# Kernel optimization log

Measured on AMD Instinct MI355X. Metric: run time of the kernel, lower is better.

## Reference

```python
import jax, jax.numpy as jnp
import numpy as np

N, E, F, H, C, K, L, B = 50000, 800000, 64, 64, 10, 4, 3, 256


def setup_inputs() -> dict:
    key = jax.random.key(0)
    ks = jax.random.split(key, 24)
    nrm = lambda k, s, sc=0.1: jax.random.normal(k, s, jnp.float32) * sc
    inp = {}
    inp['x'] = jax.random.normal(ks[0], (N, F), jnp.float32)
    inp['edge_index'] = jax.random.randint(ks[1], (2, E), 0, N)
    inp['batch'] = jnp.sort(jax.random.randint(ks[2], (N,), 0, B))
    i = 3
    for pre in ('ce', 'cl'):  # causal encoder / classifier encoder (GIN, F==H)
        inp[pre + '_W1'] = nrm(ks[i], (L, H, H)); inp[pre + '_b1'] = jnp.zeros((L, H), jnp.float32)
        inp[pre + '_W2'] = nrm(ks[i + 1], (L, H, H)); inp[pre + '_b2'] = jnp.zeros((L, H), jnp.float32)
        inp[pre + '_eps'] = jnp.zeros((L,), jnp.float32)
        i += 2
    inp['nm_W1'] = nrm(ks[i], (K, H, H)); inp['nm_b1'] = jnp.zeros((K, H), jnp.float32)
    inp['nm_W2'] = nrm(ks[i + 1], (K, H, 1)); inp['nm_b2'] = jnp.zeros((K, 1), jnp.float32)
    inp['em_W1'] = nrm(ks[i + 2], (K, 2 * H, H)); inp['em_b1'] = jnp.zeros((K, H), jnp.float32)
    inp['em_W2'] = nrm(ks[i + 3], (K, H, 1)); inp['em_b2'] = jnp.zeros((K, 1), jnp.float32)
    inp['fm_W1'] = nrm(ks[i + 4], (K, H, H)); inp['fm_b1'] = jnp.zeros((K, H), jnp.float32)
    inp['fm_W2'] = nrm(ks[i + 5], (K, H, F)); inp['fm_b2'] = jnp.zeros((K, F), jnp.float32)
    inp['clf_W'] = nrm(ks[i + 6], (K, H, C)); inp['clf_b'] = jnp.zeros((K, C), jnp.float32)
    return inp


def _gin(h, src, dst, W1, b1, W2, b2, eps, ew=None):
    """GIN with edge weights: h' = MLP((1+eps)*h + sum_j w_ij * h_j), ReLU after each conv."""
    n = h.shape[0]
    for l in range(W1.shape[0]):
        m = h[src]                                   # [E, H] gather
        if ew is not None:
            m = m * ew[:, None]
        agg = jax.ops.segment_sum(m, dst, num_segments=n)  # scatter-add
        t = (1.0 + eps[l]) * h + agg
        h = jax.nn.relu(jax.nn.relu(t @ W1[l] + b1[l]) @ W2[l] + b2[l])
    return h


def _mlp2(z, W1, b1, W2, b2):
    # z: [n, d]; per-expert 2-layer MLP -> [K, n, out]
    hdn = jax.nn.relu(jnp.einsum('nd,kdh->knh', z, W1) + b1[:, None, :])
    return jnp.einsum('knh,kho->kno', hdn, W2) + b2[:, None, :]


def _mean_pool(z, batch, nseg):
    s = jax.ops.segment_sum(z, batch, num_segments=nseg)
    cnt = jax.ops.segment_sum(jnp.ones((z.shape[-2],), z.dtype), batch, num_segments=nseg)
    return s / jnp.maximum(cnt, 1.0)[:, None]


def reference(x, edge_index, batch,
              ce_W1, ce_b1, ce_W2, ce_b2, ce_eps,
              cl_W1, cl_b1, cl_W2, cl_b2, cl_eps,
              nm_W1, nm_b1, nm_W2, nm_b2,
              em_W1, em_b1, em_W2, em_b2,
              fm_W1, fm_b1, fm_W2, fm_b2,
              clf_W, clf_b):
    src, dst = edge_index[0], edge_index[1]
    Z = _gin(x, src, dst, ce_W1, ce_b1, ce_W2, ce_b2, ce_eps)          # [N, H]
    edge_feat = jnp.concatenate([Z[src], Z[dst]], axis=1)              # [E, 2H]

    node_masks = jax.nn.sigmoid(_mlp2(Z, nm_W1, nm_b1, nm_W2, nm_b2))  # [K, N, 1]
    edge_masks = jax.nn.sigmoid(_mlp2(edge_feat, em_W1, em_b1, em_W2, em_b2))  # [K, E, 1]
    feat_masks = jax.nn.sigmoid(_mlp2(Z, fm_W1, fm_b1, fm_W2, fm_b2))  # [K, N, F]

    masked_x = x[None] * node_masks * feat_masks                       # [K, N, F]
    ew = edge_masks[..., 0]                                            # [K, E]

    masked_Z = jax.vmap(
        lambda h0, w: _gin(h0, src, dst, cl_W1, cl_b1, cl_W2, cl_b2, cl_eps, ew=w)
    )(masked_x, ew)                                                    # [K, N, H]

    h_stable = jax.vmap(lambda z: _mean_pool(z, batch, B))(masked_Z)   # [K, B, H]
    expert_logits = jnp.einsum('kbh,khc->kbc', h_stable, clf_W) + clf_b[:, None, :]
    h_orig = _mean_pool(Z, batch, B)                                   # [B, H]

    # match torch's stack(dim=1) layouts
    return (jnp.transpose(expert_logits, (1, 0, 2)),   # [B, K, C]
            jnp.transpose(h_stable, (1, 0, 2)),        # [B, K, H]
            h_orig,                                    # [B, H]
            jnp.transpose(node_masks, (1, 0, 2)),      # [N, K, 1]
            jnp.transpose(edge_masks, (1, 0, 2)),      # [E, K, 1]
            jnp.transpose(feat_masks, (1, 0, 2)))      # [N, K, F]
```

## Files before the change

kernel.cpp:

```cpp
#include <hip/hip_runtime.h>
#include <math.h>

#define N_NODES 50000
#define N_EDGES 800000
#define DIM 64
#define NB 256
#define NK 4
#define NC 10
#define TPAD 68
#define SCAN_BLKS 196

typedef unsigned int uint_;
typedef unsigned short ushort_;

__device__ __forceinline__ float sigmoidf_(float x){ return 1.f/(1.f+__expf(-x)); }
__device__ __forceinline__ float bf2f(ushort_ v){ return __uint_as_float(((uint_)v)<<16); }
__device__ __forceinline__ float bflo(uint_ u){ return __uint_as_float(u<<16); }
__device__ __forceinline__ float bfhi(uint_ u){ return __uint_as_float(u & 0xFFFF0000u); }
__device__ __forceinline__ ushort_ f2bf(float f){
    uint_ u = __float_as_uint(f);
    u = (u + 0x7FFFu + ((u>>16)&1u)) >> 16;
    return (ushort_)u;
}

__global__ void deg_hist_kernel(const int* __restrict__ ei, int* __restrict__ deg){
    int e = blockIdx.x*256 + threadIdx.x;
    if (e < N_EDGES) atomicAdd(&deg[ei[N_EDGES + e]], 1);
}

__global__ __launch_bounds__(256)
void scan_p1(const int* __restrict__ deg, int* __restrict__ rowptr, int* __restrict__ bsum){
    __shared__ int s[256];
    int tid = threadIdx.x;
    int i = blockIdx.x*256 + tid;
    int v = (i < N_NODES) ? deg[i] : 0;
    s[tid] = v;
    __syncthreads();
    for (int off = 1; off < 256; off <<= 1){
        int t = (tid >= off) ? s[tid - off] : 0;
        __syncthreads();
        s[tid] += t;
        __syncthreads();
    }
    if (i < N_NODES) rowptr[i] = s[tid] - v;
    if (tid == 255) bsum[blockIdx.x] = s[255];
}

__global__ __launch_bounds__(256)
void scan_p2(const int* __restrict__ bsum, int* __restrict__ boff){
    __shared__ int s[256];
    int tid = threadIdx.x;
    int v = (tid < SCAN_BLKS) ? bsum[tid] : 0;
    s[tid] = v;
    __syncthreads();
    for (int off = 1; off < 256; off <<= 1){
        int t = (tid >= off) ? s[tid - off] : 0;
        __syncthreads();
        s[tid] += t;
        __syncthreads();
    }
    boff[tid] = s[tid] - v;
}

__global__ __launch_bounds__(256)
void scan_p3(int* __restrict__ rowptr, const int* __restrict__ boff, int* __restrict__ cursor){
    int i = blockIdx.x*256 + threadIdx.x;
    if (i < N_NODES){
        int r = rowptr[i] + boff[blockIdx.x];
        rowptr[i] = r;
        cursor[i] = r;
    }
    if (i == 0) rowptr[N_NODES] = N_EDGES;
}

__global__ void csr_fill_kernel(const int* __restrict__ ei, int* __restrict__ cursor,
                                int* __restrict__ csr_src, int* __restrict__ csr_eid){
    int e = blockIdx.x*256 + threadIdx.x;
    if (e < N_EDGES){
        int d = ei[N_EDGES + e];
        int pos = atomicAdd(&cursor[d], 1);
        csr_src[pos] = ei[e];
        csr_eid[pos] = e;
    }
}

__global__ void tobf16_kernel(const float* __restrict__ x, ushort_* __restrict__ o){
    int i = blockIdx.x*256 + threadIdx.x;
    if (i < N_NODES*DIM/4){
        float4 v = *(const float4*)&x[(size_t)i*4];
        ushort4 o4;
        o4.x = f2bf(v.x); o4.y = f2bf(v.y); o4.z = f2bf(v.z); o4.w = f2bf(v.w);
        *(ushort4*)&o[(size_t)i*4] = o4;
    }
}

__global__ __launch_bounds__(256)
void agg_ce_kernel(const ushort_* __restrict__ hin, float* __restrict__ outt,
                   const int* __restrict__ rowptr, const int* __restrict__ csr_src,
                   const float* __restrict__ eps_p)
{
    const int n = blockIdx.x*4 + (threadIdx.x >> 6);
    if (n >= N_NODES) return;
    const int lane = threadIdx.x & 63;
    const int f2 = lane & 31;
    const int p  = lane >> 5;
    float a0 = 0.f, a1 = 0.f;
    int idx = rowptr[n];
    const int end = rowptr[n+1];
    for (; idx + 4 <= end; idx += 4){
        int e0 = idx + p*2, e1 = e0 + 1;
        int s0 = csr_src[e0], s1 = csr_src[e1];
        uint_ g0 = *(const uint_*)&hin[(size_t)s0*DIM + f2*2];
        uint_ g1 = *(const uint_*)&hin[(size_t)s1*DIM + f2*2];
        a0 += bflo(g0) + bflo(g1);
        a1 += bfhi(g0) + bfhi(g1);
    }
    for (; idx < end; idx += 2){
        int e = idx + p;
        bool v = e < end;
        int s = v ? csr_src[e] : 0;
        uint_ g = v ? *(const uint_*)&hin[(size_t)s*DIM + f2*2] : 0u;
        a0 += bflo(g);
        a1 += bfhi(g);
    }
    a0 += __shfl_xor(a0, 32);
    a1 += __shfl_xor(a1, 32);
    const float epv = 1.0f + *eps_p;
    uint_ hs = *(const uint_*)&hin[(size_t)n*DIM + f2*2];
    a0 = fmaf(epv, bflo(hs), a0);
    a1 = fmaf(epv, bfhi(hs), a1);
    if (p == 0){
        *(float2*)&outt[(size_t)n*DIM + f2*2] = make_float2(a0, a1);
    }
}

__global__ __launch_bounds__(256)
void agg4_kernel(const ushort_* __restrict__ h4, ushort_* __restrict__ out4,
                 const int* __restrict__ rowptr, const int* __restrict__ csr_src,
                 const ushort_* __restrict__ ewi, const float* __restrict__ eps_p)
{
    const int n = blockIdx.x*4 + (threadIdx.x >> 6);
    if (n >= N_NODES) return;
    const int lane = threadIdx.x & 63;
    const int k = lane >> 4;
    const float epv = 1.0f + *eps_p;
    uint2 self = *(const uint2*)&h4[(size_t)n*(NK*DIM) + lane*4];
    float c0 = epv*bflo(self.x), c1 = epv*bfhi(self.x);
    float c2 = epv*bflo(self.y), c3 = epv*bfhi(self.y);
    int idx = rowptr[n];
    const int end = rowptr[n+1];
    for (; idx + 4 <= end; idx += 4){
        int s0 = csr_src[idx+0], s1 = csr_src[idx+1];
        int s2 = csr_src[idx+2], s3 = csr_src[idx+3];
        uint2 g0 = *(const uint2*)&h4[(size_t)s0*(NK*DIM) + lane*4];
        uint2 g1 = *(const uint2*)&h4[(size_t)s1*(NK*DIM) + lane*4];
        uint2 g2 = *(const uint2*)&h4[(size_t)s2*(NK*DIM) + lane*4];
        uint2 g3 = *(const uint2*)&h4[(size_t)s3*(NK*DIM) + lane*4];
        float w0 = bf2f(ewi[(size_t)(idx+0)*NK + k]);
        float w1 = bf2f(ewi[(size_t)(idx+1)*NK + k]);
        float w2 = bf2f(ewi[(size_t)(idx+2)*NK + k]);
        float w3 = bf2f(ewi[(size_t)(idx+3)*NK + k]);
        c0 = fmaf(w0, bflo(g0.x), c0); c1 = fmaf(w0, bfhi(g0.x), c1);
        c2 = fmaf(w0, bflo(g0.y), c2); c3 = fmaf(w0, bfhi(g0.y), c3);
        c0 = fmaf(w1, bflo(g1.x), c0); c1 = fmaf(w1, bfhi(g1.x), c1);
        c2 = fmaf(w1, bflo(g1.y), c2); c3 = fmaf(w1, bfhi(g1.y), c3);
        c0 = fmaf(w2, bflo(g2.x), c0); c1 = fmaf(w2, bfhi(g2.x), c1);
        c2 = fmaf(w2, bflo(g2.y), c2); c3 = fmaf(w2, bfhi(g2.y), c3);
        c0 = fmaf(w3, bflo(g3.x), c0); c1 = fmaf(w3, bfhi(g3.x), c1);
        c2 = fmaf(w3, bflo(g3.y), c2); c3 = fmaf(w3, bfhi(g3.y), c3);
    }
    for (; idx < end; ++idx){
        int s = csr_src[idx];
        uint2 g = *(const uint2*)&h4[(size_t)s*(NK*DIM) + lane*4];
        float w = bf2f(ewi[(size_t)idx*NK + k]);
        c0 = fmaf(w, bflo(g.x), c0); c1 = fmaf(w, bfhi(g.x), c1);
        c2 = fmaf(w, bflo(g.y), c2); c3 = fmaf(w, bfhi(g.y), c3);
    }
    ushort4 o;
    o.x = f2bf(c0); o.y = f2bf(c1); o.z = f2bf(c2); o.w = f2bf(c3);
    *(ushort4*)&out4[(size_t)n*(NK*DIM) + lane*4] = o;
}

__device__ __forceinline__ void load_tileT_f32s(const float* __restrict__ in, float As[DIM][TPAD],
                                                int m0, int tid, int istride, int ibase){
    int r = tid >> 2, cq = (tid & 3) * 16;
    bool valid = (m0 + r) < N_NODES;
#pragma unroll
    for (int i = 0; i < 4; i++){
        float4 v = valid ? *(const float4*)&in[(size_t)(m0 + r)*istride + ibase + cq + 4*i]
                         : make_float4(0.f, 0.f, 0.f, 0.f);
        As[cq + 4*i + 0][r] = v.x;
        As[cq + 4*i + 1][r] = v.y;
        As[cq + 4*i + 2][r] = v.z;
        As[cq + 4*i + 3][r] = v.w;
    }
}

__device__ __forceinline__ void load_tileT_b16s(const ushort_* __restrict__ in, float As[DIM][TPAD],
                                                int m0, int tid, int istride, int ibase){
    int r = tid >> 2, cq = (tid & 3) * 16;
    bool valid = (m0 + r) < N_NODES;
    uint_ us[8] = {0,0,0,0,0,0,0,0};
    if (valid){
        const uint_* p = (const uint_*)&in[(size_t)(m0 + r)*istride + ibase + cq];
        uint4 a = *(const uint4*)p;
        uint4 b = *(const uint4*)(p + 4);
        us[0]=a.x; us[1]=a.y; us[2]=a.z; us[3]=a.w;
        us[4]=b.x; us[5]=b.y; us[6]=b.z; us[7]=b.w;
    }
#pragma unroll
    for (int w = 0; w < 8; w++){
        As[cq + 2*w + 0][r] = bflo(us[w]);
        As[cq + 2*w + 1][r] = bfhi(us[w]);
    }
}

__device__ __forceinline__ void load_w(const float* __restrict__ W, float Ws[DIM][TPAD], int tid){
    int kr = tid >> 2, cq = (tid & 3) * 16;
#pragma unroll
    for (int i = 0; i < 4; i++){
        *(float4*)&Ws[kr][cq + 4*i] = *(const float4*)&W[(size_t)kr*DIM + cq + 4*i];
    }
}

template<int IN16, int ACT2, int OUT16, int PERK_W>
__global__ __launch_bounds__(256)
void mlpX_kernel(const void* __restrict__ inp, void* __restrict__ outp,
                 const float* __restrict__ W1, const float* __restrict__ b1,
                 const float* __restrict__ W2, const float* __restrict__ b2,
                 int istride, int ibase_k, int ostride, int obase_k)
{
    __shared__ __align__(16) float As[DIM][TPAD];
    __shared__ __align__(16) float Ws[DIM][TPAD];
    __shared__ __align__(16) float Ts[DIM][TPAD];
    const int tid = threadIdx.x;
    const int tx = tid & 15, ty = tid >> 4;
    const int m0 = blockIdx.x * 64;
    const int k = blockIdx.y;
    if (PERK_W){
        W1 += (size_t)k*DIM*DIM; b1 += (size_t)k*DIM;
        W2 += (size_t)k*DIM*DIM; b2 += (size_t)k*DIM;
    }
    const int ibase = k * ibase_k;
    const size_t obase = (size_t)k * obase_k;

    if (IN16) load_tileT_b16s((const ushort_*)inp, As, m0, tid, istride, ibase);
    else      load_tileT_f32s((const float*)inp, As, m0, tid, istride, ibase);
    load_w(W1, Ws, tid);
    __syncthreads();

    float acc[4][4];
    {
        float4 b1v = *(const float4*)&b1[tx*4];
        float bv[4] = {b1v.x, b1v.y, b1v.z, b1v.w};
#pragma unroll
        for (int i = 0; i < 4; i++)
#pragma unroll
            for (int j = 0; j < 4; j++) acc[i][j] = bv[j];
    }
#pragma unroll 8
    for (int kk = 0; kk < DIM; kk++){
        float4 a = *(const float4*)&As[kk][ty*4];
        float4 w = *(const float4*)&Ws[kk][tx*4];
        float av[4] = {a.x, a.y, a.z, a.w};
        float wv[4] = {w.x, w.y, w.z, w.w};
#pragma unroll
        for (int i = 0; i < 4; i++)
#pragma unroll
            for (int j = 0; j < 4; j++) acc[i][j] = fmaf(av[i], wv[j], acc[i][j]);
    }
#pragma unroll
    for (int j = 0; j < 4; j++){
        float4 v = make_float4(fmaxf(acc[0][j],0.f), fmaxf(acc[1][j],0.f),
                               fmaxf(acc[2][j],0.f), fmaxf(acc[3][j],0.f));
        *(float4*)&Ts[tx*4 + j][ty*4] = v;
    }
    __syncthreads();
    load_w(W2, Ws, tid);
    __syncthreads();

    float acc2[4][4];
    {
        float4 b2v = *(const float4*)&b2[tx*4];
        float bv[4] = {b2v.x, b2v.y, b2v.z, b2v.w};
#pragma unroll
        for (int i = 0; i < 4; i++)
#pragma unroll
            for (int j = 0; j < 4; j++) acc2[i][j] = bv[j];
    }
#pragma unroll 8
    for (int kk = 0; kk < DIM; kk++){
        float4 a = *(const float4*)&Ts[kk][ty*4];
        float4 w = *(const float4*)&Ws[kk][tx*4];
        float av[4] = {a.x, a.y, a.z, a.w};
        float wv[4] = {w.x, w.y, w.z, w.w};
#pragma unroll
        for (int i = 0; i < 4; i++)
#pragma unroll
            for (int j = 0; j < 4; j++) acc2[i][j] = fmaf(av[i], wv[j], acc2[i][j]);
    }
#pragma unroll
    for (int i = 0; i < 4; i++){
        int m = m0 + ty*4 + i;
        if (m < N_NODES){
            float v0, v1, v2, v3;
            if (ACT2 == 0){
                v0 = fmaxf(acc2[i][0],0.f); v1 = fmaxf(acc2[i][1],0.f);
                v2 = fmaxf(acc2[i][2],0.f); v3 = fmaxf(acc2[i][3],0.f);
            } else {
                v0 = sigmoidf_(acc2[i][0]); v1 = sigmoidf_(acc2[i][1]);
                v2 = sigmoidf_(acc2[i][2]); v3 = sigmoidf_(acc2[i][3]);
            }
            if (OUT16){
                ushort4 o;
                o.x = f2bf(v0); o.y = f2bf(v1); o.z = f2bf(v2); o.w = f2bf(v3);
                *(ushort4*)&((ushort_*)outp)[obase + (size_t)m*ostride + tx*4] = o;
            } else {
                *(float4*)&((float*)outp)[obase + (size_t)m*ostride + tx*4] =
                    make_float4(v0, v1, v2, v3);
            }
        }
    }
}

__global__ __launch_bounds__(256)
void nm4_kernel(const ushort_* __restrict__ Z16, float* __restrict__ nm_out,
                const float* __restrict__ nmW1, const float* __restrict__ nmb1,
                const float* __restrict__ nmW2, const float* __restrict__ nmb2)
{
    __shared__ __align__(16) float As[DIM][TPAD];
    __shared__ __align__(16) float Ws[DIM][TPAD];
    __shared__ __align__(16) float Ts[DIM][TPAD];
    __shared__ float w2s[DIM];
    __shared__ float red[4][DIM];
    const int tid = threadIdx.x;
    const int tx = tid & 15, ty = tid >> 4;
    const int m0 = blockIdx.x * 64;
    const int k = blockIdx.y;
    const float* W1 = nmW1 + (size_t)k*DIM*DIM;
    const float* b1 = nmb1 + (size_t)k*DIM;
    const float* w2 = nmW2 + (size_t)k*DIM;

    load_tileT_b16s(Z16, As, m0, tid, DIM, 0);
    load_w(W1, Ws, tid);
    if (tid < DIM) w2s[tid] = w2[tid];
    __syncthreads();

    float acc[4][4];
    {
        float4 b1v = *(const float4*)&b1[tx*4];
        float bv[4] = {b1v.x, b1v.y, b1v.z, b1v.w};
#pragma unroll
        for (int i = 0; i < 4; i++)
#pragma unroll
            for (int j = 0; j < 4; j++) acc[i][j] = bv[j];
    }
#pragma unroll 8
    for (int kk = 0; kk < DIM; kk++){
        float4 a = *(const float4*)&As[kk][ty*4];
        float4 w = *(const float4*)&Ws[kk][tx*4];
        float av[4] = {a.x, a.y, a.z, a.w};
        float wv[4] = {w.x, w.y, w.z, w.w};
#pragma unroll
        for (int i = 0; i < 4; i++)
#pragma unroll
            for (int j = 0; j < 4; j++) acc[i][j] = fmaf(av[i], wv[j], acc[i][j]);
    }
#pragma unroll
    for (int j = 0; j < 4; j++){
        float4 v = make_float4(fmaxf(acc[0][j],0.f), fmaxf(acc[1][j],0.f),
                               fmaxf(acc[2][j],0.f), fmaxf(acc[3][j],0.f));
        *(float4*)&Ts[tx*4 + j][ty*4] = v;
    }
    __syncthreads();
    {
        int m = tid & 63, q = tid >> 6;
        float p = 0.f;
#pragma unroll
        for (int kk = 0; kk < 16; kk++) p = fmaf(Ts[q*16 + kk][m], w2s[q*16 + kk], p);
        red[q][m] = p;
    }
    __syncthreads();
    if (tid < DIM){
        int m = m0 + tid;
        if (m < N_NODES){
            float sm = red[0][tid] + red[1][tid] + red[2][tid] + red[3][tid] + nmb2[k];
            nm_out[(size_t)m*NK + k] = sigmoidf_(sm);
        }
    }
}

__global__ __launch_bounds__(256)
void em_proj4_kernel(const ushort_* __restrict__ Z16, const float* __restrict__ emW1,
                     ushort_* __restrict__ pt4, ushort_* __restrict__ pb4)
{
    __shared__ __align__(16) float As[DIM][TPAD];
    __shared__ __align__(16) float Ws[DIM][TPAD];
    const int s = blockIdx.y;
    const int k = s >> 1, side = s & 1;
    const float* W = emW1 + ((size_t)k*2 + side)*DIM*DIM;
    ushort_* outp = side ? pb4 : pt4;
    const int tid = threadIdx.x;
    const int tx = tid & 15, ty = tid >> 4;
    const int m0 = blockIdx.x * 64;

    load_tileT_b16s(Z16, As, m0, tid, DIM, 0);
    load_w(W, Ws, tid);
    __syncthreads();

    float acc[4][4] = {};
#pragma unroll 8
    for (int kk = 0; kk < DIM; kk++){
        float4 a = *(const float4*)&As[kk][ty*4];
        float4 w = *(const float4*)&Ws[kk][tx*4];
        float av[4] = {a.x, a.y, a.z, a.w};
        float wv[4] = {w.x, w.y, w.z, w.w};
#pragma unroll
        for (int i = 0; i < 4; i++)
#pragma unroll
            for (int j = 0; j < 4; j++) acc[i][j] = fmaf(av[i], wv[j], acc[i][j]);
    }
#pragma unroll
    for (int i = 0; i < 4; i++){
        int m = m0 + ty*4 + i;
        if (m < N_NODES){
            ushort4 o;
            o.x = f2bf(acc[i][0]); o.y = f2bf(acc[i][1]);
            o.z = f2bf(acc[i][2]); o.w = f2bf(acc[i][3]);
            *(ushort4*)&outp[(size_t)m*(NK*DIM) + k*DIM + tx*4] = o;
        }
    }
}

__global__ __launch_bounds__(256)
void edge_mask16_kernel(const ushort_* __restrict__ pt4, const ushort_* __restrict__ pb4,
                        const int* __restrict__ rowptr, const int* __restrict__ csr_src,
                        const int* __restrict__ csr_eid,
                        const float* __restrict__ emb1, const float* __restrict__ emW2,
                        const float* __restrict__ emb2,
                        float* __restrict__ em_out, ushort_* __restrict__ ewi)
{
    const int n = blockIdx.x*4 + (threadIdx.x >> 6);
    if (n >= N_NODES) return;
    const int lane = threadIdx.x & 63;
    const int k = lane >> 4, fq = lane & 15;
    const float4 w2v = *(const float4*)&emW2[k*DIM + fq*4];
    const float4 b1v = *(const float4*)&emb1[k*DIM + fq*4];
    const float b2 = emb2[k];
    uint2 pbu = *(const uint2*)&pb4[(size_t)n*(NK*DIM) + k*DIM + fq*4];
    const float pre0 = bflo(pbu.x) + b1v.x;
    const float pre1 = bfhi(pbu.x) + b1v.y;
    const float pre2 = bflo(pbu.y) + b1v.z;
    const float pre3 = bfhi(pbu.y) + b1v.w;
    int i = rowptr[n];
    const int end = rowptr[n+1];
    for (; i + 2 <= end; i += 2){
        int s0 = csr_src[i], s1 = csr_src[i+1];
        uint2 a0 = *(const uint2*)&pt4[(size_t)s0*(NK*DIM) + k*DIM + fq*4];
        uint2 a1 = *(const uint2*)&pt4[(size_t)s1*(NK*DIM) + k*DIM + fq*4];
        float p0 = fmaxf(bflo(a0.x) + pre0, 0.f)*w2v.x + fmaxf(bfhi(a0.x) + pre1, 0.f)*w2v.y
                 + fmaxf(bflo(a0.y) + pre2, 0.f)*w2v.z + fmaxf(bfhi(a0.y) + pre3, 0.f)*w2v.w;
        float p1 = fmaxf(bflo(a1.x) + pre0, 0.f)*w2v.x + fmaxf(bfhi(a1.x) + pre1, 0.f)*w2v.y
                 + fmaxf(bflo(a1.y) + pre2, 0.f)*w2v.z + fmaxf(bfhi(a1.y) + pre3, 0.f)*w2v.w;
        p0 += __shfl_xor(p0, 1, 16); p1 += __shfl_xor(p1, 1, 16);
        p0 += __shfl_xor(p0, 2, 16); p1 += __shfl_xor(p1, 2, 16);
        p0 += __shfl_xor(p0, 4, 16); p1 += __shfl_xor(p1, 4, 16);
        p0 += __shfl_xor(p0, 8, 16); p1 += __shfl_xor(p1, 8, 16);
        if (fq == 0){
            float m0v = sigmoidf_(p0 + b2);
            float m1v = sigmoidf_(p1 + b2);
            em_out[(size_t)csr_eid[i]*NK + k]   = m0v;
            em_out[(size_t)csr_eid[i+1]*NK + k] = m1v;
            ewi[(size_t)i*NK + k]     = f2bf(m0v);
            ewi[(size_t)(i+1)*NK + k] = f2bf(m1v);
        }
    }
    for (; i < end; ++i){
        int s0 = csr_src[i];
        uint2 a0 = *(const uint2*)&pt4[(size_t)s0*(NK*DIM) + k*DIM + fq*4];
        float p0 = fmaxf(bflo(a0.x) + pre0, 0.f)*w2v.x + fmaxf(bfhi(a0.x) + pre1, 0.f)*w2v.y
                 + fmaxf(bflo(a0.y) + pre2, 0.f)*w2v.z + fmaxf(bfhi(a0.y) + pre3, 0.f)*w2v.w;
        p0 += __shfl_xor(p0, 1, 16);
        p0 += __shfl_xor(p0, 2, 16);
        p0 += __shfl_xor(p0, 4, 16);
        p0 += __shfl_xor(p0, 8, 16);
        if (fq == 0){
            float m0v = sigmoidf_(p0 + b2);
            em_out[(size_t)csr_eid[i]*NK + k] = m0v;
            ewi[(size_t)i*NK + k] = f2bf(m0v);
        }
    }
}

__global__ void build_h04_kernel(const float* __restrict__ x, const float* __restrict__ nm_out,
                                 const float* __restrict__ fm_out, ushort_* __restrict__ h4)
{
    int t = blockIdx.x*256 + threadIdx.x;
    if (t < N_NODES*64){
        int n = t >> 6;
        int q = t & 63;
        int k = q >> 4, c = (q & 15) * 4;
        float nm = nm_out[(size_t)n*NK + k];
        float4 xv = *(const float4*)&x[(size_t)n*DIM + c];
        float4 fv = *(const float4*)&fm_out[((size_t)n*NK + k)*DIM + c];
        ushort4 o;
        o.x = f2bf(xv.x*nm*fv.x); o.y = f2bf(xv.y*nm*fv.y);
        o.z = f2bf(xv.z*nm*fv.z); o.w = f2bf(xv.w*nm*fv.w);
        *(ushort4*)&h4[(size_t)n*(NK*DIM) + k*DIM + c] = o;
    }
}

__device__ __forceinline__ int lower_bound_(const int* a, int n, int v){
    int lo = 0, hi = n;
    while (lo < hi){ int m = (lo + hi) >> 1; if (a[m] < v) lo = m + 1; else hi = m; }
    return lo;
}

__global__ __launch_bounds__(64)
void pool_orig_kernel(const ushort_* __restrict__ h, const int* __restrict__ batch, float* __restrict__ out){
    int b = blockIdx.x, lane = threadIdx.x;
    int lo = lower_bound_(batch, N_NODES, b);
    int hi = lower_bound_(batch, N_NODES, b+1);
    float s = 0.f;
    int n = lo;
    for (; n + 4 <= hi; n += 4){
        s += bf2f(h[(size_t)n*DIM + lane]) + bf2f(h[(size_t)(n+1)*DIM + lane])
           + bf2f(h[(size_t)(n+2)*DIM + lane]) + bf2f(h[(size_t)(n+3)*DIM + lane]);
    }
    for (; n < hi; ++n) s += bf2f(h[(size_t)n*DIM + lane]);
    out[(size_t)b*DIM + lane] = s / fmaxf((float)(hi - lo), 1.f);
}

__global__ __launch_bounds__(64)
void pool4_kernel(const ushort_* __restrict__ h4, const int* __restrict__ batch,
                  const float* __restrict__ clfW, const float* __restrict__ clfb,
                  float* __restrict__ out_logits, float* __restrict__ out_hst)
{
    __shared__ float ms[DIM];
    int b = blockIdx.x, k = blockIdx.y, lane = threadIdx.x;
    int lo = lower_bound_(batch, N_NODES, b);
    int hi = lower_bound_(batch, N_NODES, b+1);
    const ushort_* h = h4 + (size_t)k*DIM;
    float s = 0.f;
    int n = lo;
    for (; n + 4 <= hi; n += 4){
        s += bf2f(h[(size_t)n*(NK*DIM) + lane]) + bf2f(h[(size_t)(n+1)*(NK*DIM) + lane])
           + bf2f(h[(size_t)(n+2)*(NK*DIM) + lane]) + bf2f(h[(size_t)(n+3)*(NK*DIM) + lane]);
    }
    for (; n < hi; ++n) s += bf2f(h[(size_t)n*(NK*DIM) + lane]);
    float m = s / fmaxf((float)(hi - lo), 1.f);
    out_hst[((size_t)b*NK + k)*DIM + lane] = m;
    ms[lane] = m;
    __syncthreads();
    if (lane < NC){
        float a = clfb[(size_t)k*NC + lane];
        const float* W = clfW + (size_t)k*DIM*NC;
#pragma unroll
        for (int j = 0; j < DIM; j++) a = fmaf(ms[j], W[j*NC + lane], a);
        out_logits[((size_t)b*NK + k)*NC + lane] = a;
    }
}

extern "C" void kernel_launch(void* const* d_in, const int* in_sizes, int n_in,
                              void* d_out, int out_size, void* d_ws, size_t ws_size,
                              hipStream_t stream)
{
    const float* x     = (const float*)d_in[0];
    const int*   ei    = (const int*)  d_in[1];
    const int*   batch = (const int*)  d_in[2];
    const float* ceW1 = (const float*)d_in[3];
    const float* ceb1 = (const float*)d_in[4];
    const float* ceW2 = (const float*)d_in[5];
    const float* ceb2 = (const float*)d_in[6];
    const float* ceeps= (const float*)d_in[7];
    const float* clW1 = (const float*)d_in[8];
    const float* clb1 = (const float*)d_in[9];
    const float* clW2 = (const float*)d_in[10];
    const float* clb2 = (const float*)d_in[11];
    const float* cleps= (const float*)d_in[12];
    const float* nmW1 = (const float*)d_in[13];
    const float* nmb1 = (const float*)d_in[14];
    const float* nmW2 = (const float*)d_in[15];
    const float* nmb2 = (const float*)d_in[16];
    const float* emW1 = (const float*)d_in[17];
    const float* emb1 = (const float*)d_in[18];
    const float* emW2 = (const float*)d_in[19];
    const float* emb2 = (const float*)d_in[20];
    const float* fmW1 = (const float*)d_in[21];
    const float* fmb1 = (const float*)d_in[22];
    const float* fmW2 = (const float*)d_in[23];
    const float* fmb2 = (const float*)d_in[24];
    const float* clfW = (const float*)d_in[25];
    const float* clfb = (const float*)d_in[26];

    float* out        = (float*)d_out;
    float* out_logits = out;
    float* out_hst    = out + 10240;
    float* out_horig  = out + 75776;
    float* nm_out     = out + 92160;
    float* em_out     = out + 292160;
    float* fm_out     = out + 3492160;

    int* rowptr  = (int*)d_ws;
    int* cursor  = rowptr + (N_NODES + 1);
    int* deg     = cursor + N_NODES;
    int* csr_src = deg + N_NODES;
    int* csr_eid = csr_src + N_EDGES;
    int* bsum    = csr_eid + N_EDGES;
    int* boff    = bsum + 256;
    size_t int_count = (size_t)(N_NODES+1) + N_NODES + N_NODES + N_EDGES + N_EDGES + 512;
    int_count = (int_count + 3) & ~(size_t)3;
    const size_t ND = (size_t)N_NODES*DIM;
    float*   tbuf = (float*)(((int*)d_ws) + int_count);
    ushort_* hx16 = (ushort_*)(tbuf + ND);
    ushort_* TA   = hx16 + ND;
    ushort_* h4A  = (ushort_*)tbuf;
    ushort_* TB   = TA + ND;
    ushort_* pt4  = TB + ND;
    ushort_* pb4  = pt4 + ND*NK;
    ushort_* ewi  = pb4 + ND*NK;
    ushort_* t16  = pt4;
    ushort_* h4B  = pb4;

    const int GT = (N_NODES + 63) / 64;
    const int GW = (N_NODES + 3) / 4;

    hipMemsetAsync(deg, 0, N_NODES*sizeof(int), stream);
    deg_hist_kernel<<<(N_EDGES+255)/256, 256, 0, stream>>>(ei, deg);
    scan_p1<<<SCAN_BLKS, 256, 0, stream>>>(deg, rowptr, bsum);
    scan_p2<<<1, 256, 0, stream>>>(bsum, boff);
    scan_p3<<<SCAN_BLKS, 256, 0, stream>>>(rowptr, boff, cursor);
    csr_fill_kernel<<<(N_EDGES+255)/256, 256, 0, stream>>>(ei, cursor, csr_src, csr_eid);

    tobf16_kernel<<<(N_NODES*DIM/4+255)/256, 256, 0, stream>>>(x, hx16);

    agg_ce_kernel<<<GW, 256, 0, stream>>>(hx16, tbuf, rowptr, csr_src, ceeps + 0);
    mlpX_kernel<0,0,1,0><<<dim3(GT,1), 256, 0, stream>>>(tbuf, TA, ceW1 + 0*DIM*DIM, ceb1 + 0*DIM,
                                                         ceW2 + 0*DIM*DIM, ceb2 + 0*DIM, DIM, 0, DIM, 0);
    agg_ce_kernel<<<GW, 256, 0, stream>>>(TA, tbuf, rowptr, csr_src, ceeps + 1);
    mlpX_kernel<0,0,1,0><<<dim3(GT,1), 256, 0, stream>>>(tbuf, TB, ceW1 + 1*DIM*DIM, ceb1 + 1*DIM,
                                                         ceW2 + 1*DIM*DIM, ceb2 + 1*DIM, DIM, 0, DIM, 0);
    agg_ce_kernel<<<GW, 256, 0, stream>>>(TB, tbuf, rowptr, csr_src, ceeps + 2);
    mlpX_kernel<0,0,1,0><<<dim3(GT,1), 256, 0, stream>>>(tbuf, TA, ceW1 + 2*DIM*DIM, ceb1 + 2*DIM,
                                                         ceW2 + 2*DIM*DIM, ceb2 + 2*DIM, DIM, 0, DIM, 0);
    const ushort_* Z16 = TA;

    pool_orig_kernel<<<NB, 64, 0, stream>>>(Z16, batch, out_horig);

    em_proj4_kernel<<<dim3(GT, 2*NK), 256, 0, stream>>>(Z16, emW1, pt4, pb4);
    edge_mask16_kernel<<<GW, 256, 0, stream>>>(pt4, pb4, rowptr, csr_src, csr_eid,
                                               emb1, emW2, emb2, em_out, ewi);

    nm4_kernel<<<dim3(GT, NK), 256, 0, stream>>>(Z16, nm_out, nmW1, nmb1, nmW2, nmb2);
    mlpX_kernel<1,1,0,1><<<dim3(GT, NK), 256, 0, stream>>>(Z16, fm_out, fmW1, fmb1, fmW2, fmb2,
                                                           DIM, 0, NK*DIM, DIM);

    build_h04_kernel<<<(N_NODES*64+255)/256, 256, 0, stream>>>(x, nm_out, fm_out, h4A);

    agg4_kernel<<<GW, 256, 0, stream>>>(h4A, t16, rowptr, csr_src, ewi, cleps + 0);
    mlpX_kernel<1,0,1,0><<<dim3(GT, NK), 256, 0, stream>>>(t16, h4B, clW1 + 0*DIM*DIM, clb1 + 0*DIM,
                                                           clW2 + 0*DIM*DIM, clb2 + 0*DIM,
                                                           NK*DIM, DIM, NK*DIM, DIM);
    agg4_kernel<<<GW, 256, 0, stream>>>(h4B, t16, rowptr, csr_src, ewi, cleps + 1);
    mlpX_kernel<1,0,1,0><<<dim3(GT, NK), 256, 0, stream>>>(t16, h4A, clW1 + 1*DIM*DIM, clb1 + 1*DIM,
                                                           clW2 + 1*DIM*DIM, clb2 + 1*DIM,
                                                           NK*DIM, DIM, NK*DIM, DIM);
    agg4_kernel<<<GW, 256, 0, stream>>>(h4A, t16, rowptr, csr_src, ewi, cleps + 2);
    mlpX_kernel<1,0,1,0><<<dim3(GT, NK), 256, 0, stream>>>(t16, h4B, clW1 + 2*DIM*DIM, clb1 + 2*DIM,
                                                           clW2 + 2*DIM*DIM, clb2 + 2*DIM,
                                                           NK*DIM, DIM, NK*DIM, DIM);

    pool4_kernel<<<dim3(NB, NK), 64, 0, stream>>>(h4B, batch, clfW, clfb, out_logits, out_hst);
}
```

Measured before the change: 995.4 us.

## Store gathered node features and edge projections in FP8 instead of BF16

The per-expert node features gathered by the classifier GIN aggregation, the edge-mask projection tables and the pooled final hidden states are now written as packed FP8 (four values per 32-bit word). They are unpacked with the hardware cvt_pk_f32_fp8 instructions. This halves the bytes moved by the random-access gathers in agg4 and edge_mask, which are likely bandwidth or latency bound. The trade-off is a large loss of precision (FP8 mantissa) in intermediate activations, which may break accuracy tolerance. The workspace layout is also reshuffled so h4B gets its own region.

```diff
diff --git a/kernel.cpp b/kernel.cpp
--- a/kernel.cpp
+++ b/kernel.cpp
@@ -12,6 +12,8 @@
 
 typedef unsigned int uint_;
 typedef unsigned short ushort_;
+typedef unsigned char uchar_;
+typedef float f32x2_ __attribute__((ext_vector_type(2)));
 
 __device__ __forceinline__ float sigmoidf_(float x){ return 1.f/(1.f+__expf(-x)); }
 __device__ __forceinline__ float bf2f(ushort_ v){ return __uint_as_float(((uint_)v)<<16); }
@@ -21,6 +23,13 @@
     uint_ u = __float_as_uint(f);
     u = (u + 0x7FFFu + ((u>>16)&1u)) >> 16;
     return (ushort_)u;
+}
+__device__ __forceinline__ f32x2_ fp8lo(uint_ u){ return __builtin_amdgcn_cvt_pk_f32_fp8(u, false); }
+__device__ __forceinline__ f32x2_ fp8hi(uint_ u){ return __builtin_amdgcn_cvt_pk_f32_fp8(u, true); }
+__device__ __forceinline__ uint_ pack_fp8x4(float a, float b, float c, float d){
+    uint_ u = __builtin_amdgcn_cvt_pk_fp8_f32(a, b, 0, false);
+    u = __builtin_amdgcn_cvt_pk_fp8_f32(c, d, u, true);
+    return u;
 }
 
 __global__ void deg_hist_kernel(const int* __restrict__ ei, int* __restrict__ deg){
@@ -135,7 +144,7 @@
 }
 
 __global__ __launch_bounds__(256)
-void agg4_kernel(const ushort_* __restrict__ h4, ushort_* __restrict__ out4,
+void agg4_kernel(const uint_* __restrict__ h4, ushort_* __restrict__ out4,
                  const int* __restrict__ rowptr, const int* __restrict__ csr_src,
                  const ushort_* __restrict__ ewi, const float* __restrict__ eps_p)
 {
@@ -144,37 +153,42 @@
     const int lane = threadIdx.x & 63;
     const int k = lane >> 4;
     const float epv = 1.0f + *eps_p;
-    uint2 self = *(const uint2*)&h4[(size_t)n*(NK*DIM) + lane*4];
-    float c0 = epv*bflo(self.x), c1 = epv*bfhi(self.x);
-    float c2 = epv*bflo(self.y), c3 = epv*bfhi(self.y);
+    uint_ self = h4[(size_t)n*64 + lane];
+    f32x2_ sl = fp8lo(self), sh = fp8hi(self);
+    float c0 = epv*sl.x, c1 = epv*sl.y, c2 = epv*sh.x, c3 = epv*sh.y;
     int idx = rowptr[n];
     const int end = rowptr[n+1];
     for (; idx + 4 <= end; idx += 4){
         int s0 = csr_src[idx+0], s1 = csr_src[idx+1];
         int s2 = csr_src[idx+2], s3 = csr_src[idx+3];
-        uint2 g0 = *(const uint2*)&h4[(size_t)s0*(NK*DIM) + lane*4];
-        uint2 g1 = *(const uint2*)&h4[(size_t)s1*(NK*DIM) + lane*4];
-        uint2 g2 = *(const uint2*)&h4[(size_t)s2*(NK*DIM) + lane*4];
-        uint2 g3 = *(const uint2*)&h4[(size_t)s3*(NK*DIM) + lane*4];
+        uint_ g0 = h4[(size_t)s0*64 + lane];
+        uint_ g1 = h4[(size_t)s1*64 + lane];
+        uint_ g2 = h4[(size_t)s2*64 + lane];
+        uint_ g3 = h4[(size_t)s3*64 + lane];
         float w0 = bf2f(ewi[(size_t)(idx+0)*NK + k]);
         float w1 = bf2f(ewi[(size_t)(idx+1)*NK + k]);
         float w2 = bf2f(ewi[(size_t)(idx+2)*NK + k]);
         float w3 = bf2f(ewi[(size_t)(idx+3)*NK + k]);
-        c0 = fmaf(w0, bflo(g0.x), c0); c1 = fmaf(w0, bfhi(g0.x), c1);
-        c2 = fmaf(w0, bflo(g0.y), c2); c3 = fmaf(w0, bfhi(g0.y), c3);
-        c0 = fmaf(w1, bflo(g1.x), c0); c1 = fmaf(w1, bfhi(g1.x), c1);
-        c2 = fmaf(w1, bflo(g1.y), c2); c3 = fmaf(w1, bfhi(g1.y), c3);
-        c0 = fmaf(w2, bflo(g2.x), c0); c1 = fmaf(w2, bfhi(g2.x), c1);
-        c2 = fmaf(w2, bflo(g2.y), c2); c3 = fmaf(w2, bfhi(g2.y), c3);
-        c0 = fmaf(w3, bflo(g3.x), c0); c1 = fmaf(w3, bfhi(g3.x), c1);
-        c2 = fmaf(w3, bflo(g3.y), c2); c3 = fmaf(w3, bfhi(g3.y), c3);
+        f32x2_ l0 = fp8lo(g0), h0v = fp8hi(g0);
+        f32x2_ l1 = fp8lo(g1), h1v = fp8hi(g1);
+        f32x2_ l2 = fp8lo(g2), h2v = fp8hi(g2);
+        f32x2_ l3 = fp8lo(g3), h3v = fp8hi(g3);
+        c0 = fmaf(w0, l0.x, c0); c1 = fmaf(w0, l0.y, c1);
+        c2 = fmaf(w0, h0v.x, c2); c3 = fmaf(w0, h0v.y, c3);
+        c0 = fmaf(w1, l1.x, c0); c1 = fmaf(w1, l1.y, c1);
+        c2 = fmaf(w1, h1v.x, c2); c3 = fmaf(w1, h1v.y, c3);
+        c0 = fmaf(w2, l2.x, c0); c1 = fmaf(w2, l2.y, c1);
+        c2 = fmaf(w2, h2v.x, c2); c3 = fmaf(w2, h2v.y, c3);
+        c0 = fmaf(w3, l3.x, c0); c1 = fmaf(w3, l3.y, c1);
+        c2 = fmaf(w3, h3v.x, c2); c3 = fmaf(w3, h3v.y, c3);
     }
     for (; idx < end; ++idx){
         int s = csr_src[idx];
-        uint2 g = *(const uint2*)&h4[(size_t)s*(NK*DIM) + lane*4];
+        uint_ g = h4[(size_t)s*64 + lane];
         float w = bf2f(ewi[(size_t)idx*NK + k]);
-        c0 = fmaf(w, bflo(g.x), c0); c1 = fmaf(w, bfhi(g.x), c1);
-        c2 = fmaf(w, bflo(g.y), c2); c3 = fmaf(w, bfhi(g.y), c3);
+        f32x2_ l = fp8lo(g), h = fp8hi(g);
+        c0 = fmaf(w, l.x, c0); c1 = fmaf(w, l.y, c1);
+        c2 = fmaf(w, h.x, c2); c3 = fmaf(w, h.y, c3);
     }
     ushort4 o;
     o.x = f2bf(c0); o.y = f2bf(c1); o.z = f2bf(c2); o.w = f2bf(c3);
@@ -223,7 +237,7 @@
     }
 }
 
-template<int IN16, int ACT2, int OUT16, int PERK_W>
+template<int IN16, int ACT2, int OUTMODE, int PERK_W>
 __global__ __launch_bounds__(256)
 void mlpX_kernel(const void* __restrict__ inp, void* __restrict__ outp,
                  const float* __restrict__ W1, const float* __restrict__ b1,
@@ -311,10 +325,13 @@
                 v0 = sigmoidf_(acc2[i][0]); v1 = sigmoidf_(acc2[i][1]);
                 v2 = sigmoidf_(acc2[i][2]); v3 = sigmoidf_(acc2[i][3]);
             }
-            if (OUT16){
+            if (OUTMODE == 1){
                 ushort4 o;
                 o.x = f2bf(v0); o.y = f2bf(v1); o.z = f2bf(v2); o.w = f2bf(v3);
                 *(ushort4*)&((ushort_*)outp)[obase + (size_t)m*ostride + tx*4] = o;
+            } else if (OUTMODE == 2){
+                uint_ u = pack_fp8x4(v0, v1, v2, v3);
+                ((uint_*)outp)[(obase >> 2) + (size_t)m*(ostride >> 2) + tx] = u;
             } else {
                 *(float4*)&((float*)outp)[obase + (size_t)m*ostride + tx*4] =
                     make_float4(v0, v1, v2, v3);
@@ -392,14 +409,14 @@
 
 __global__ __launch_bounds__(256)
 void em_proj4_kernel(const ushort_* __restrict__ Z16, const float* __restrict__ emW1,
-                     ushort_* __restrict__ pt4, ushort_* __restrict__ pb4)
+                     uint_* __restrict__ pt4, uint_* __restrict__ pb4)
 {
     __shared__ __align__(16) float As[DIM][TPAD];
     __shared__ __align__(16) float Ws[DIM][TPAD];
     const int s = blockIdx.y;
     const int k = s >> 1, side = s & 1;
     const float* W = emW1 + ((size_t)k*2 + side)*DIM*DIM;
-    ushort_* outp = side ? pb4 : pt4;
+    uint_* outp = side ? pb4 : pt4;
     const int tid = threadIdx.x;
     const int tx = tid & 15, ty = tid >> 4;
     const int m0 = blockIdx.x * 64;
@@ -424,16 +441,13 @@
     for (int i = 0; i < 4; i++){
         int m = m0 + ty*4 + i;
         if (m < N_NODES){
-            ushort4 o;
-            o.x = f2bf(acc[i][0]); o.y = f2bf(acc[i][1]);
-            o.z = f2bf(acc[i][2]); o.w = f2bf(acc[i][3]);
-            *(ushort4*)&outp[(size_t)m*(NK*DIM) + k*DIM + tx*4] = o;
+            outp[(size_t)m*64 + k*16 + tx] = pack_fp8x4(acc[i][0], acc[i][1], acc[i][2], acc[i][3]);
         }
     }
 }
 
 __global__ __launch_bounds__(256)
-void edge_mask16_kernel(const ushort_* __restrict__ pt4, const ushort_* __restrict__ pb4,
+void edge_mask16_kernel(const uint_* __restrict__ pt4, const uint_* __restrict__ pb4,
                         const int* __restrict__ rowptr, const int* __restrict__ csr_src,
                         const int* __restrict__ csr_eid,
                         const float* __restrict__ emb1, const float* __restrict__ emW2,
@@ -447,21 +461,24 @@
     const float4 w2v = *(const float4*)&emW2[k*DIM + fq*4];
     const float4 b1v = *(const float4*)&emb1[k*DIM + fq*4];
     const float b2 = emb2[k];
-    uint2 pbu = *(const uint2*)&pb4[(size_t)n*(NK*DIM) + k*DIM + fq*4];
-    const float pre0 = bflo(pbu.x) + b1v.x;
-    const float pre1 = bfhi(pbu.x) + b1v.y;
-    const float pre2 = bflo(pbu.y) + b1v.z;
-    const float pre3 = bfhi(pbu.y) + b1v.w;
+    uint_ pbu = pb4[(size_t)n*64 + k*16 + fq];
+    f32x2_ plo = fp8lo(pbu), phi = fp8hi(pbu);
+    const float pre0 = plo.x + b1v.x;
+    const float pre1 = plo.y + b1v.y;
+    const float pre2 = phi.x + b1v.z;
+    const float pre3 = phi.y + b1v.w;
     int i = rowptr[n];
     const int end = rowptr[n+1];
     for (; i + 2 <= end; i += 2){
         int s0 = csr_src[i], s1 = csr_src[i+1];
-        uint2 a0 = *(const uint2*)&pt4[(size_t)s0*(NK*DIM) + k*DIM + fq*4];
-        uint2 a1 = *(const uint2*)&pt4[(size_t)s1*(NK*DIM) + k*DIM + fq*4];
-        float p0 = fmaxf(bflo(a0.x) + pre0, 0.f)*w2v.x + fmaxf(bfhi(a0.x) + pre1, 0.f)*w2v.y
-                 + fmaxf(bflo(a0.y) + pre2, 0.f)*w2v.z + fmaxf(bfhi(a0.y) + pre3, 0.f)*w2v.w;
-        float p1 = fmaxf(bflo(a1.x) + pre0, 0.f)*w2v.x + fmaxf(bfhi(a1.x) + pre1, 0.f)*w2v.y
-                 + fmaxf(bflo(a1.y) + pre2, 0.f)*w2v.z + fmaxf(bfhi(a1.y) + pre3, 0.f)*w2v.w;
+        uint_ a0 = pt4[(size_t)s0*64 + k*16 + fq];
+        uint_ a1 = pt4[(size_t)s1*64 + k*16 + fq];
+        f32x2_ a0l = fp8lo(a0), a0h = fp8hi(a0);
+        f32x2_ a1l = fp8lo(a1), a1h = fp8hi(a1);
+        float p0 = fmaxf(a0l.x + pre0, 0.f)*w2v.x + fmaxf(a0l.y + pre1, 0.f)*w2v.y
+                 + fmaxf(a0h.x + pre2, 0.f)*w2v.z + fmaxf(a0h.y + pre3, 0.f)*w2v.w;
+        float p1 = fmaxf(a1l.x + pre0, 0.f)*w2v.x + fmaxf(a1l.y + pre1, 0.f)*w2v.y
+                 + fmaxf(a1h.x + pre2, 0.f)*w2v.z + fmaxf(a1h.y + pre3, 0.f)*w2v.w;
         p0 += __shfl_xor(p0, 1, 16); p1 += __shfl_xor(p1, 1, 16);
         p0 += __shfl_xor(p0, 2, 16); p1 += __shfl_xor(p1, 2, 16);
         p0 += __shfl_xor(p0, 4, 16); p1 += __shfl_xor(p1, 4, 16);
@@ -477,9 +494,10 @@
     }
     for (; i < end; ++i){
         int s0 = csr_src[i];
-        uint2 a0 = *(const uint2*)&pt4[(size_t)s0*(NK*DIM) + k*DIM + fq*4];
-        float p0 = fmaxf(bflo(a0.x) + pre0, 0.f)*w2v.x + fmaxf(bfhi(a0.x) + pre1, 0.f)*w2v.y
-                 + fmaxf(bflo(a0.y) + pre2, 0.f)*w2v.z + fmaxf(bfhi(a0.y) + pre3, 0.f)*w2v.w;
+        uint_ a0 = pt4[(size_t)s0*64 + k*16 + fq];
+        f32x2_ a0l = fp8lo(a0), a0h = fp8hi(a0);
+        float p0 = fmaxf(a0l.x + pre0, 0.f)*w2v.x + fmaxf(a0l.y + pre1, 0.f)*w2v.y
+                 + fmaxf(a0h.x + pre2, 0.f)*w2v.z + fmaxf(a0h.y + pre3, 0.f)*w2v.w;
         p0 += __shfl_xor(p0, 1, 16);
         p0 += __shfl_xor(p0, 2, 16);
         p0 += __shfl_xor(p0, 4, 16);
@@ -493,7 +511,7 @@
 }
 
 __global__ void build_h04_kernel(const float* __restrict__ x, const float* __restrict__ nm_out,
-                                 const float* __restrict__ fm_out, ushort_* __restrict__ h4)
+                                 const float* __restrict__ fm_out, uint_* __restrict__ h4)
 {
     int t = blockIdx.x*256 + threadIdx.x;
     if (t < N_NODES*64){
@@ -503,10 +521,8 @@
         float nm = nm_out[(size_t)n*NK + k];
         float4 xv = *(const float4*)&x[(size_t)n*DIM + c];
         float4 fv = *(const float4*)&fm_out[((size_t)n*NK + k)*DIM + c];
-        ushort4 o;
-        o.x = f2bf(xv.x*nm*fv.x); o.y = f2bf(xv.y*nm*fv.y);
-        o.z = f2bf(xv.z*nm*fv.z); o.w = f2bf(xv.w*nm*fv.w);
-        *(ushort4*)&h4[(size_t)n*(NK*DIM) + k*DIM + c] = o;
+        h4[(size_t)n*64 + q] = pack_fp8x4(xv.x*nm*fv.x, xv.y*nm*fv.y,
+                                          xv.z*nm*fv.z, xv.w*nm*fv.w);
     }
 }
 
@@ -532,7 +548,7 @@
 }
 
 __global__ __launch_bounds__(64)
-void pool4_kernel(const ushort_* __restrict__ h4, const int* __restrict__ batch,
+void pool4_kernel(const uint_* __restrict__ h4, const int* __restrict__ batch,
                   const float* __restrict__ clfW, const float* __restrict__ clfb,
                   float* __restrict__ out_logits, float* __restrict__ out_hst)
 {
@@ -540,14 +556,16 @@
     int b = blockIdx.x, k = blockIdx.y, lane = threadIdx.x;
     int lo = lower_bound_(batch, N_NODES, b);
     int hi = lower_bound_(batch, N_NODES, b+1);
-    const ushort_* h = h4 + (size_t)k*DIM;
+    const uchar_* h = (const uchar_*)h4 + (size_t)k*DIM + lane;
     float s = 0.f;
     int n = lo;
     for (; n + 4 <= hi; n += 4){
-        s += bf2f(h[(size_t)n*(NK*DIM) + lane]) + bf2f(h[(size_t)(n+1)*(NK*DIM) + lane])
-           + bf2f(h[(size_t)(n+2)*(NK*DIM) + lane]) + bf2f(h[(size_t)(n+3)*(NK*DIM) + lane]);
-    }
-    for (; n < hi; ++n) s += bf2f(h[(size_t)n*(NK*DIM) + lane]);
+        s += __builtin_amdgcn_cvt_f32_fp8((uint_)h[(size_t)n*256], 0)
+           + __builtin_amdgcn_cvt_f32_fp8((uint_)h[(size_t)(n+1)*256], 0)
+           + __builtin_amdgcn_cvt_f32_fp8((uint_)h[(size_t)(n+2)*256], 0)
+           + __builtin_amdgcn_cvt_f32_fp8((uint_)h[(size_t)(n+3)*256], 0);
+    }
+    for (; n < hi; ++n) s += __builtin_amdgcn_cvt_f32_fp8((uint_)h[(size_t)n*256], 0);
     float m = s / fmaxf((float)(hi - lo), 1.f);
     out_hst[((size_t)b*NK + k)*DIM + lane] = m;
     ms[lane] = m;
@@ -614,13 +632,13 @@
     float*   tbuf = (float*)(((int*)d_ws) + int_count);
     ushort_* hx16 = (ushort_*)(tbuf + ND);
     ushort_* TA   = hx16 + ND;
-    ushort_* h4A  = (ushort_*)tbuf;
+    uint_*   h4A  = (uint_*)tbuf;
     ushort_* TB   = TA + ND;
-    ushort_* pt4  = TB + ND;
-    ushort_* pb4  = pt4 + ND*NK;
-    ushort_* ewi  = pb4 + ND*NK;
-    ushort_* t16  = pt4;
-    ushort_* h4B  = pb4;
+    uint_*   pt4  = (uint_*)(TB + ND);
+    uint_*   pb4  = pt4 + (size_t)N_NODES*64;
+    ushort_* t16  = (ushort_*)pt4;
+    ushort_* ewi  = (ushort_*)(pb4 + (size_t)N_NODES*64);
+    uint_*   h4B  = (uint_*)(ewi + (size_t)N_EDGES*NK);
 
     const int GT = (N_NODES + 63) / 64;
     const int GW = (N_NODES + 3) / 4;
@@ -658,15 +676,15 @@
     build_h04_kernel<<<(N_NODES*64+255)/256, 256, 0, stream>>>(x, nm_out, fm_out, h4A);
 
     agg4_kernel<<<GW, 256, 0, stream>>>(h4A, t16, rowptr, csr_src, ewi, cleps + 0);
-    mlpX_kernel<1,0,1,0><<<dim3(GT, NK), 256, 0, stream>>>(t16, h4B, clW1 + 0*DIM*DIM, clb1 + 0*DIM,
+    mlpX_kernel<1,0,2,0><<<dim3(GT, NK), 256, 0, stream>>>(t16, h4B, clW1 + 0*DIM*DIM, clb1 + 0*DIM,
                                                            clW2 + 0*DIM*DIM, clb2 + 0*DIM,
                                                            NK*DIM, DIM, NK*DIM, DIM);
     agg4_kernel<<<GW, 256, 0, stream>>>(h4B, t16, rowptr, csr_src, ewi, cleps + 1);
-    mlpX_kernel<1,0,1,0><<<dim3(GT, NK), 256, 0, stream>>>(t16, h4A, clW1 + 1*DIM*DIM, clb1 + 1*DIM,
+    mlpX_kernel<1,0,2,0><<<dim3(GT, NK), 256, 0, stream>>>(t16, h4A, clW1 + 1*DIM*DIM, clb1 + 1*DIM,
                                                            clW2 + 1*DIM*DIM, clb2 + 1*DIM,
                                                            NK*DIM, DIM, NK*DIM, DIM);
     agg4_kernel<<<GW, 256, 0, stream>>>(h4A, t16, rowptr, csr_src, ewi, cleps + 2);
-    mlpX_kernel<1,0,1,0><<<dim3(GT, NK), 256, 0, stream>>>(t16, h4B, clW1 + 2*DIM*DIM, clb1 + 2*DIM,
+    mlpX_kernel<1,0,2,0><<<dim3(GT, NK), 256, 0, stream>>>(t16, h4B, clW1 + 2*DIM*DIM, clb1 + 2*DIM,
                                                            clW2 + 2*DIM*DIM, clb2 + 2*DIM,
                                                            NK*DIM, DIM, NK*DIM, DIM);
 
```

Result: faster. 909.8 us (-8.6%).
